# Kernel tuning notes

Hardware: AMD Instinct MI355X
Metric: run time of the kernel (lower is better)

The kernel has to match this reference:

```python
import jax, jax.numpy as jnp
import numpy as np

N_NODES = 50000
N_EDGES = 1_280_000
NODE_D = 13
EDGE_RAW_D = 1
H = 64
CONCAT_D = 2 * NODE_D + EDGE_RAW_D  # 27
NEG_SLOPE = 0.2


def _leaky(x):
    return jnp.where(x >= 0, x, NEG_SLOPE * x)


def _scatter_mean(vals, idx, num_nodes):
    # vals: [E, H]; idx: [E] int -> [num_nodes, H] mean over incident edges (0 if none)
    s = jax.ops.segment_sum(vals, idx, num_segments=num_nodes)
    cnt = jax.ops.segment_sum(jnp.ones((vals.shape[0], 1), vals.dtype), idx, num_segments=num_nodes)
    return s / jnp.maximum(cnt, 1.0)


def _conv(e, src, dst, num_nodes, w_self, b_self, w_in, w_out):
    h_self = e @ w_self + b_self
    agg_in = _scatter_mean(e, dst, num_nodes)[src]   # incoming-edge mean at src nodes
    agg_out = _scatter_mean(e, src, num_nodes)[dst]  # outgoing-edge mean at dst nodes
    return _leaky(h_self + agg_in @ w_in + agg_out @ w_out)


def setup_inputs() -> dict:
    key = jax.random.key(0)
    ks = jax.random.split(key, 24)

    def lin(k, fan_in, fan_out):
        return jax.random.normal(k, (fan_in, fan_out), jnp.float32) / np.sqrt(fan_in)

    inp = {
        'x': jax.random.normal(ks[0], (N_NODES, NODE_D), jnp.float32),
        'edge_index': jax.random.randint(ks[1], (2, N_EDGES), 0, N_NODES, jnp.int32),
        'raw_edge_attr': jax.random.normal(ks[2], (N_EDGES, EDGE_RAW_D), jnp.float32),
        'enc_w': lin(ks[3], CONCAT_D, H),
        'enc_b': jnp.zeros((H,), jnp.float32),
    }
    for i, base in zip((1, 2, 3), (4, 8, 12)):
        inp[f'w_self{i}'] = lin(ks[base], H, H)
        inp[f'b_self{i}'] = jnp.zeros((H,), jnp.float32)
        inp[f'w_in{i}'] = lin(ks[base + 1], H, H)
        inp[f'w_out{i}'] = lin(ks[base + 2], H, H)
    dims = [(H, 64), (64, 64), (64, 32), (32, 1)]
    for j, (fi, fo) in enumerate(dims, start=1):
        inp[f'mlp_w{j}'] = lin(ks[15 + j], fi, fo)
        inp[f'mlp_b{j}'] = jnp.zeros((fo,), jnp.float32)
    return inp


def reference(x, edge_index, raw_edge_attr, enc_w, enc_b,
              w_self1, b_self1, w_in1, w_out1,
              w_self2, b_self2, w_in2, w_out2,
              w_self3, b_self3, w_in3, w_out3,
              mlp_w1, mlp_b1, mlp_w2, mlp_b2, mlp_w3, mlp_b3, mlp_w4, mlp_b4):
    num_nodes = x.shape[0]
    src, dst = edge_index[0], edge_index[1]
    edge_attr = jnp.concatenate([x[src], x[dst], raw_edge_attr], axis=-1)  # [E, 27]
    h = _leaky(edge_attr @ enc_w + enc_b)
    h = _conv(h, src, dst, num_nodes, w_self1, b_self1, w_in1, w_out1)
    h = _conv(h, src, dst, num_nodes, w_self2, b_self2, w_in2, w_out2)
    h = _conv(h, src, dst, num_nodes, w_self3, b_self3, w_in3, w_out3)
    h = _leaky(h @ mlp_w1 + mlp_b1)
    h = _leaky(h @ mlp_w2 + mlp_b2)
    h = _leaky(h @ mlp_w3 + mlp_b3)
    return (h @ mlp_w4 + mlp_b4).squeeze(-1)  # [E]
```

## Files before the change

kernel.cpp:

```cpp
#include <hip/hip_runtime.h>


#define NN 50000
#define NNP 50048
#define NE 1280000
#define LDP 72
#define NB 196
#define NTILES 782
#define NPX 6250
#define CAP 64

#define WAVES 2
#define EDGE_ITERS 4
#define EDGE_BLOCKS 2500
#define ENC_ITERS 2
#define ENC_BLOCKS 5000

typedef unsigned int   u32;
typedef unsigned short u16;
typedef __attribute__((ext_vector_type(8))) short  short8;
typedef __attribute__((ext_vector_type(4))) float  floatx4;

#define MFMA16(a, b, c) __builtin_amdgcn_mfma_f32_16x16x32_bf16(a, b, c, 0, 0, 0)

__device__ __forceinline__ float lrelu(float x) { return fmaxf(x, 0.2f * x); }
__device__ __forceinline__ float bf2f(u16 u) { return __uint_as_float(((u32)u) << 16); }
__device__ __forceinline__ u16 f2bf(float f) {
    u32 b = __float_as_uint(f);
    return (u16)((b + 0x7FFFu + ((b >> 16) & 1u)) >> 16);
}
__device__ __forceinline__ u32 f2bf2(float lo, float hi) {
    u32 r;
    asm("v_cvt_pk_bf16_f32 %0, %1, %2" : "=v"(r) : "v"(lo), "v"(hi));
    return r;
}
__device__ __forceinline__ void ub2(u32 w, float& lo, float& hi) {
    lo = __uint_as_float(w << 16);
    hi = __uint_as_float(w & 0xFFFF0000u);
}

__device__ __forceinline__ short8 bfragP(const float* __restrict__ W, int ld, int n, int k0) {
    short8 b;
#pragma unroll
    for (int j = 0; j < 8; ++j) {
        const int p = k0 + j;
        const int k = (p & 3) * 16 + (p >> 2);
        b[j] = (short)f2bf(W[k * ld + n]);
    }
    return b;
}

__device__ __forceinline__ void mm_tile(const u16* __restrict__ tb,
                                        const short8 wf[2][4],
                                        floatx4 acc[4][4], int c16, int q4) {
#pragma unroll
    for (int mt = 0; mt < 4; ++mt) {
        const short8 a0 = *(const short8*)(tb + (mt * 16 + c16) * LDP + q4 * 8);
        const short8 a1 = *(const short8*)(tb + (mt * 16 + c16) * LDP + 32 + q4 * 8);
#pragma unroll
        for (int nt = 0; nt < 4; ++nt) {
            acc[mt][nt] = MFMA16(a0, wf[0][nt], acc[mt][nt]);
            acc[mt][nt] = MFMA16(a1, wf[1][nt], acc[mt][nt]);
        }
    }
}

__global__ void __launch_bounds__(256)
k_prep(const float* __restrict__ x, u16* __restrict__ xb)
{
    const int n = blockIdx.x * 256 + threadIdx.x;
    if (n >= NN) return;
    float f[13];
#pragma unroll
    for (int j = 0; j < 13; ++j) f[j] = x[n * 13 + j];
    uint4 p0, p1;
    p0.x = f2bf2(f[0],  f[1]);  p0.y = f2bf2(f[2],  f[3]);
    p0.z = f2bf2(f[4],  f[5]);  p0.w = f2bf2(f[6],  f[7]);
    p1.x = f2bf2(f[8],  f[9]);  p1.y = f2bf2(f[10], f[11]);
    p1.z = f2bf2(f[12], 0.0f);  p1.w = 0u;
    *(uint4*)(xb + (size_t)n * 16)     = p0;
    *(uint4*)(xb + (size_t)n * 16 + 8) = p1;
}

__global__ void __launch_bounds__(256)
k_fill(const int* __restrict__ ei, int* __restrict__ cnt_in, int* __restrict__ cnt_out,
       int* __restrict__ csr_in, int* __restrict__ csr_out)
{
    const int cls   = blockIdx.x & 7;
    const int slice = blockIdx.x >> 3;
    const int base  = (slice * 256 + threadIdx.x) * 8;
    const int lo = cls * NPX, hi = lo + NPX;
    int s[8], d[8];
#pragma unroll
    for (int k = 0; k < 8; ++k) s[k] = ei[base + k];
#pragma unroll
    for (int k = 0; k < 8; ++k) d[k] = ei[NE + base + k];
#pragma unroll
    for (int k = 0; k < 8; ++k)
        if (s[k] >= lo && s[k] < hi) {
            const int p = atomicAdd(&cnt_out[s[k]], 1);
            if (p < CAP) csr_out[s[k] * CAP + p] = base + k;
        }
#pragma unroll
    for (int k = 0; k < 8; ++k)
        if (d[k] >= lo && d[k] < hi) {
            const int q = atomicAdd(&cnt_in[d[k]], 1);
            if (q < CAP) csr_in[d[k] * CAP + q] = base + k;
        }
}

__global__ void __launch_bounds__(128)
k_enc(const u16* __restrict__ xb, const int* __restrict__ ei,
      const float* __restrict__ raw, const float* __restrict__ wenc,
      const float* __restrict__ benc, u16* __restrict__ hm)
{
    __shared__ int sidx[WAVES][64], didx[WAVES][64];
    const int w = threadIdx.x >> 6, lane = threadIdx.x & 63;
    const int c16 = lane & 15, q4 = lane >> 4;

    short8 wf[4];
    float bias[4];
#pragma unroll
    for (int nt = 0; nt < 4; ++nt) {
        short8 b;
#pragma unroll
        for (int j = 0; j < 8; ++j) {
            const int p = q4 * 8 + j;
            int row;
            if (p < 13)                 row = p;
            else if (p == 13)           row = 26;
            else if (p >= 16 && p < 29) row = 13 + (p - 16);
            else                        row = -1;
            b[j] = (short)(row >= 0 ? f2bf(wenc[row * 64 + nt * 16 + c16]) : 0);
        }
        wf[nt] = b;
        bias[nt] = benc[nt * 16 + c16];
    }

    for (int it = 0; it < ENC_ITERS; ++it) {
        const int tileId = (it * ENC_BLOCKS + blockIdx.x) * WAVES + w;
        const int e0 = tileId * 64;

        sidx[w][lane] = ei[e0 + lane];
        didx[w][lane] = ei[NE + e0 + lane];

#pragma unroll
        for (int mt = 0; mt < 4; ++mt) {
            const int arow = mt * 16 + c16;
            const int* nbase = (q4 < 2) ? sidx[w] : didx[w];
            const int node = nbase[arow];
            short8 a = *(const short8*)(xb + (size_t)node * 16 + (q4 & 1) * 8);
            const float rv = raw[e0 + arow];
            if (q4 == 1) a[5] = (short)(u16)f2bf2(rv, 0.0f);

            floatx4 acc[4];
#pragma unroll
            for (int nt = 0; nt < 4; ++nt) acc[nt] = (floatx4)(0.0f);
#pragma unroll
            for (int nt = 0; nt < 4; ++nt) acc[nt] = MFMA16(a, wf[nt], acc[nt]);
#pragma unroll
            for (int r = 0; r < 4; ++r) {
                const int rowi = mt * 16 + q4 * 4 + r;
                uint2 pkt;
                pkt.x = f2bf2(lrelu(acc[0][r] + bias[0]), lrelu(acc[1][r] + bias[1]));
                pkt.y = f2bf2(lrelu(acc[2][r] + bias[2]), lrelu(acc[3][r] + bias[3]));
                *(uint2*)(hm + (size_t)(e0 + rowi) * 64 + c16 * 4) = pkt;
            }
        }
    }
}

__global__ void __launch_bounds__(256)
k_mean(const u16* __restrict__ hm,
       const int* __restrict__ cnt_in, const int* __restrict__ csr_in,
       const int* __restrict__ cnt_out, const int* __restrict__ csr_out,
       u16* __restrict__ m_in, u16* __restrict__ m_out)
{
    const int w = threadIdx.x >> 6, lane = threadIdx.x & 63;
    const int node = blockIdx.x * 4 + w;
    const int rg = lane >> 3;
    const int co = (lane & 7) * 8;

    for (int pass = 0; pass < 2; ++pass) {
        const int* cnt = pass ? cnt_out : cnt_in;
        const int* csr = pass ? csr_out : csr_in;
        u16* mp        = pass ? m_out : m_in;

        const int deg = min(cnt[node], CAP);
        const int b0 = node * CAP, b1 = b0 + deg;
        float fa[8], fb[8];
#pragma unroll
        for (int c = 0; c < 8; ++c) { fa[c] = 0.f; fb[c] = 0.f; }

        int j = b0;
        for (; j + 16 <= b1; j += 16) {
            const int ea = csr[j + rg];
            const int eb = csr[j + 8 + rg];
            const uint4 va = *(const uint4*)(hm + (size_t)ea * 64 + co);
            const uint4 vb = *(const uint4*)(hm + (size_t)eb * 64 + co);
            float l0, h0, l1, h1, l2, h2, l3, h3;
            ub2(va.x, l0, h0); ub2(va.y, l1, h1); ub2(va.z, l2, h2); ub2(va.w, l3, h3);
            fa[0] += l0; fa[1] += h0; fa[2] += l1; fa[3] += h1;
            fa[4] += l2; fa[5] += h2; fa[6] += l3; fa[7] += h3;
            ub2(vb.x, l0, h0); ub2(vb.y, l1, h1); ub2(vb.z, l2, h2); ub2(vb.w, l3, h3);
            fb[0] += l0; fb[1] += h0; fb[2] += l1; fb[3] += h1;
            fb[4] += l2; fb[5] += h2; fb[6] += l3; fb[7] += h3;
        }
        for (; j < b1; j += 8) {
            const int jj = j + rg;
            const int idx = jj < b1 ? jj : b0;
            const float fl = jj < b1 ? 1.f : 0.f;
            const int e = csr[idx];
            const uint4 v = *(const uint4*)(hm + (size_t)e * 64 + co);
            float l0, h0, l1, h1, l2, h2, l3, h3;
            ub2(v.x, l0, h0); ub2(v.y, l1, h1); ub2(v.z, l2, h2); ub2(v.w, l3, h3);
            fa[0] += fl * l0; fa[1] += fl * h0; fa[2] += fl * l1; fa[3] += fl * h1;
            fa[4] += fl * l2; fa[5] += fl * h2; fa[6] += fl * l3; fa[7] += fl * h3;
        }
#pragma unroll
        for (int c = 0; c < 8; ++c) fa[c] += fb[c];
#pragma unroll
        for (int d = 8; d < 64; d <<= 1)
#pragma unroll
            for (int c = 0; c < 8; ++c) fa[c] += __shfl_xor(fa[c], d, 64);

        const float inv = 1.0f / (float)(deg > 0 ? deg : 1);
        if (lane < 8) {
            uint4 p;
            p.x = f2bf2(fa[0] * inv, fa[1] * inv);
            p.y = f2bf2(fa[2] * inv, fa[3] * inv);
            p.z = f2bf2(fa[4] * inv, fa[5] * inv);
            p.w = f2bf2(fa[6] * inv, fa[7] * inv);
            *(uint4*)(mp + (size_t)node * 64 + lane * 8) = p;
        }
    }
}

__global__ void __launch_bounds__(256)
k_nodemm(u16* t_in, u16* t_out,
         const float* __restrict__ w_in, const float* __restrict__ w_out)
{
    const int w = threadIdx.x >> 6, lane = threadIdx.x & 63;
    const int c16 = lane & 15, q4 = lane >> 4;
    const int tileId = blockIdx.x * 4 + w;
    if (tileId >= NTILES) return;
    const int n0 = tileId * 64;

    for (int pass = 0; pass < 2; ++pass) {
        u16* tp         = pass ? t_out : t_in;
        const float* wp = pass ? w_out : w_in;

        short8 wf[2][4];
#pragma unroll
        for (int ks = 0; ks < 2; ++ks)
#pragma unroll
            for (int nt = 0; nt < 4; ++nt)
                wf[ks][nt] = bfragP(wp, 64, nt * 16 + c16, ks * 32 + q4 * 8);

#pragma unroll
        for (int mt = 0; mt < 4; ++mt) {
            const short8* ap = (const short8*)(tp + (size_t)(n0 + mt * 16 + c16) * 64 + q4 * 8);
            const short8 a0 = ap[0];
            const short8 a1 = ap[4];
            floatx4 acc[4];
#pragma unroll
            for (int nt = 0; nt < 4; ++nt) acc[nt] = (floatx4)(0.0f);
#pragma unroll
            for (int nt = 0; nt < 4; ++nt) {
                acc[nt] = MFMA16(a0, wf[0][nt], acc[nt]);
                acc[nt] = MFMA16(a1, wf[1][nt], acc[nt]);
            }
#pragma unroll
            for (int r = 0; r < 4; ++r) {
                const int node = n0 + mt * 16 + q4 * 4 + r;
                if (node < NN) {
                    uint2 pkt;
                    pkt.x = f2bf2(acc[0][r], acc[1][r]);
                    pkt.y = f2bf2(acc[2][r], acc[3][r]);
                    *(uint2*)(tp + (size_t)node * 64 + c16 * 4) = pkt;
                }
            }
        }
    }
}

__global__ void __launch_bounds__(128, 4)
k_edge(const float* __restrict__ wself, const float* __restrict__ bself,
       const u16* __restrict__ t_in, const u16* __restrict__ t_out,
       const int* __restrict__ ei, u16* __restrict__ hm)
{
    __shared__ int sidx[WAVES][64], didx[WAVES][64];
    const int w = threadIdx.x >> 6, lane = threadIdx.x & 63;
    const int c16 = lane & 15, q4 = lane >> 4;

    short8 wf[2][4];
    float bias[4];
#pragma unroll
    for (int ks = 0; ks < 2; ++ks)
#pragma unroll
        for (int nt = 0; nt < 4; ++nt)
            wf[ks][nt] = bfragP(wself, 64, nt * 16 + c16, ks * 32 + q4 * 8);
#pragma unroll
    for (int nt = 0; nt < 4; ++nt) bias[nt] = bself[nt * 16 + c16];

    for (int it = 0; it < EDGE_ITERS; ++it) {
        const int tileId = (it * EDGE_BLOCKS + blockIdx.x) * WAVES + w;
        const int e0 = tileId * 64;
        sidx[w][lane] = ei[e0 + lane];
        didx[w][lane] = ei[NE + e0 + lane];

#pragma unroll
        for (int mt = 0; mt < 4; ++mt) {
            const short8* ap = (const short8*)(hm + (size_t)(e0 + mt * 16 + c16) * 64 + q4 * 8);
            const short8 a0 = ap[0];
            const short8 a1 = ap[4];
            floatx4 acc[4];
#pragma unroll
            for (int nt = 0; nt < 4; ++nt) acc[nt] = (floatx4)(0.0f);
#pragma unroll
            for (int nt = 0; nt < 4; ++nt) {
                acc[nt] = MFMA16(a0, wf[0][nt], acc[nt]);
                acc[nt] = MFMA16(a1, wf[1][nt], acc[nt]);
            }
            float tv[4][4], uv[4][4];
#pragma unroll
            for (int r = 0; r < 4; ++r) {
                const int s = sidx[w][mt * 16 + q4 * 4 + r];
                const uint2 v = *(const uint2*)(t_in + (size_t)s * 64 + c16 * 4);
                ub2(v.x, tv[r][0], tv[r][1]); ub2(v.y, tv[r][2], tv[r][3]);
            }
#pragma unroll
            for (int r = 0; r < 4; ++r) {
                const int d = didx[w][mt * 16 + q4 * 4 + r];
                const uint2 v = *(const uint2*)(t_out + (size_t)d * 64 + c16 * 4);
                ub2(v.x, uv[r][0], uv[r][1]); ub2(v.y, uv[r][2], uv[r][3]);
            }
#pragma unroll
            for (int r = 0; r < 4; ++r) {
                const int row = mt * 16 + q4 * 4 + r;
                const float v0 = lrelu(acc[0][r] + bias[0] + tv[r][0] + uv[r][0]);
                const float v1 = lrelu(acc[1][r] + bias[1] + tv[r][1] + uv[r][1]);
                const float v2 = lrelu(acc[2][r] + bias[2] + tv[r][2] + uv[r][2]);
                const float v3 = lrelu(acc[3][r] + bias[3] + tv[r][3] + uv[r][3]);
                uint2 pkt; pkt.x = f2bf2(v0, v1); pkt.y = f2bf2(v2, v3);
                *(uint2*)(hm + (size_t)(e0 + row) * 64 + c16 * 4) = pkt;
            }
        }
    }
}

__global__ void __launch_bounds__(128, 2)
k_edge_mlp(const float* __restrict__ wself, const float* __restrict__ bself,
           const u16* __restrict__ t_in, const u16* __restrict__ t_out,
           const int* __restrict__ ei, const u16* __restrict__ hm,
           const float* __restrict__ w1, const float* __restrict__ b1,
           const float* __restrict__ w2, const float* __restrict__ b2,
           const float* __restrict__ w3, const float* __restrict__ b3,
           const float* __restrict__ w4, const float* __restrict__ b4,
           float* __restrict__ out)
{
    __shared__ alignas(16) u16 tile[WAVES][64 * LDP];
    __shared__ int sidx[WAVES][64], didx[WAVES][64];
    const int w = threadIdx.x >> 6, lane = threadIdx.x & 63;
    const int c16 = lane & 15, q4 = lane >> 4;

    short8 wfS[2][4], wf1[2][4], wf2[2][4], wf3[2][2];
    float bS[4], bv1[4], bv2[4], bv3[2];
#pragma unroll
    for (int ks = 0; ks < 2; ++ks) {
#pragma unroll
        for (int nt = 0; nt < 4; ++nt) {
            wfS[ks][nt] = bfragP(wself, 64, nt * 16 + c16, ks * 32 + q4 * 8);
            wf1[ks][nt] = bfragP(w1,    64, nt * 16 + c16, ks * 32 + q4 * 8);
            wf2[ks][nt] = bfragP(w2,    64, nt * 16 + c16, ks * 32 + q4 * 8);
        }
#pragma unroll
        for (int nt = 0; nt < 2; ++nt)
            wf3[ks][nt] = bfragP(w3, 32, nt * 16 + c16, ks * 32 + q4 * 8);
    }
#pragma unroll
    for (int nt = 0; nt < 4; ++nt) { bS[nt] = bself[nt*16+c16]; bv1[nt] = b1[nt*16+c16]; bv2[nt] = b2[nt*16+c16]; }
#pragma unroll
    for (int nt = 0; nt < 2; ++nt) bv3[nt] = b3[nt * 16 + c16];
    const float w4a = w4[c16], w4b = w4[16 + c16], b4v = b4[0];

    for (int it = 0; it < EDGE_ITERS; ++it) {
        const int tileId = (it * EDGE_BLOCKS + blockIdx.x) * WAVES + w;
        const int e0 = tileId * 64;
        sidx[w][lane] = ei[e0 + lane];
        didx[w][lane] = ei[NE + e0 + lane];

#pragma unroll
        for (int mt = 0; mt < 4; ++mt) {
            const short8* ap = (const short8*)(hm + (size_t)(e0 + mt * 16 + c16) * 64 + q4 * 8);
            const short8 a0 = ap[0];
            const short8 a1 = ap[4];
            floatx4 acc[4];
#pragma unroll
            for (int nt = 0; nt < 4; ++nt) acc[nt] = (floatx4)(0.0f);
#pragma unroll
            for (int nt = 0; nt < 4; ++nt) {
                acc[nt] = MFMA16(a0, wfS[0][nt], acc[nt]);
                acc[nt] = MFMA16(a1, wfS[1][nt], acc[nt]);
            }
            float tv[4][4], uv[4][4];
#pragma unroll
            for (int r = 0; r < 4; ++r) {
                const int s = sidx[w][mt * 16 + q4 * 4 + r];
                const uint2 v = *(const uint2*)(t_in + (size_t)s * 64 + c16 * 4);
                ub2(v.x, tv[r][0], tv[r][1]); ub2(v.y, tv[r][2], tv[r][3]);
            }
#pragma unroll
            for (int r = 0; r < 4; ++r) {
                const int d = didx[w][mt * 16 + q4 * 4 + r];
                const uint2 v = *(const uint2*)(t_out + (size_t)d * 64 + c16 * 4);
                ub2(v.x, uv[r][0], uv[r][1]); ub2(v.y, uv[r][2], uv[r][3]);
            }
#pragma unroll
            for (int r = 0; r < 4; ++r) {
                const int row = mt * 16 + q4 * 4 + r;
                const float v0 = lrelu(acc[0][r] + bS[0] + tv[r][0] + uv[r][0]);
                const float v1 = lrelu(acc[1][r] + bS[1] + tv[r][1] + uv[r][1]);
                const float v2 = lrelu(acc[2][r] + bS[2] + tv[r][2] + uv[r][2]);
                const float v3 = lrelu(acc[3][r] + bS[3] + tv[r][3] + uv[r][3]);
                uint2 pkt; pkt.x = f2bf2(v0, v1); pkt.y = f2bf2(v2, v3);
                *(uint2*)(tile[w] + row * LDP + c16 * 4) = pkt;
            }
        }

        floatx4 acc[4][4];
#pragma unroll
        for (int mt = 0; mt < 4; ++mt)
#pragma unroll
            for (int nt = 0; nt < 4; ++nt) acc[mt][nt] = (floatx4)(0.0f);
        mm_tile(tile[w], wf1, acc, c16, q4);
#pragma unroll
        for (int mt = 0; mt < 4; ++mt)
#pragma unroll
            for (int r = 0; r < 4; ++r) {
                const int row = mt * 16 + q4 * 4 + r;
                uint2 pkt;
                pkt.x = f2bf2(lrelu(acc[mt][0][r] + bv1[0]), lrelu(acc[mt][1][r] + bv1[1]));
                pkt.y = f2bf2(lrelu(acc[mt][2][r] + bv1[2]), lrelu(acc[mt][3][r] + bv1[3]));
                *(uint2*)(tile[w] + row * LDP + c16 * 4) = pkt;
            }

#pragma unroll
        for (int mt = 0; mt < 4; ++mt)
#pragma unroll
            for (int nt = 0; nt < 4; ++nt) acc[mt][nt] = (floatx4)(0.0f);
        mm_tile(tile[w], wf2, acc, c16, q4);
#pragma unroll
        for (int mt = 0; mt < 4; ++mt)
#pragma unroll
            for (int r = 0; r < 4; ++r) {
                const int row = mt * 16 + q4 * 4 + r;
                uint2 pkt;
                pkt.x = f2bf2(lrelu(acc[mt][0][r] + bv2[0]), lrelu(acc[mt][1][r] + bv2[1]));
                pkt.y = f2bf2(lrelu(acc[mt][2][r] + bv2[2]), lrelu(acc[mt][3][r] + bv2[3]));
                *(uint2*)(tile[w] + row * LDP + c16 * 4) = pkt;
            }

        floatx4 a3[4][2];
#pragma unroll
        for (int mt = 0; mt < 4; ++mt)
#pragma unroll
            for (int nt = 0; nt < 2; ++nt) a3[mt][nt] = (floatx4)(0.0f);
#pragma unroll
        for (int mt = 0; mt < 4; ++mt) {
            const short8 a0 = *(const short8*)(tile[w] + (mt * 16 + c16) * LDP + q4 * 8);
            const short8 a1 = *(const short8*)(tile[w] + (mt * 16 + c16) * LDP + 32 + q4 * 8);
#pragma unroll
            for (int nt = 0; nt < 2; ++nt) {
                a3[mt][nt] = MFMA16(a0, wf3[0][nt], a3[mt][nt]);
                a3[mt][nt] = MFMA16(a1, wf3[1][nt], a3[mt][nt]);
            }
        }
#pragma unroll
        for (int mt = 0; mt < 4; ++mt)
#pragma unroll
            for (int r = 0; r < 4; ++r) {
                float p = lrelu(a3[mt][0][r] + bv3[0]) * w4a
                        + lrelu(a3[mt][1][r] + bv3[1]) * w4b;
                p += __shfl_xor(p, 1, 64);
                p += __shfl_xor(p, 2, 64);
                p += __shfl_xor(p, 4, 64);
                p += __shfl_xor(p, 8, 64);
                if (c16 == 0) out[e0 + mt * 16 + q4 * 4 + r] = p + b4v;
            }
    }
}

extern "C" void kernel_launch(void* const* d_in, const int* in_sizes, int n_in,
                              void* d_out, int out_size, void* d_ws, size_t ws_size,
                              hipStream_t stream)
{
    const float* x      = (const float*)d_in[0];
    const int*   ei     = (const int*)  d_in[1];
    const float* raw    = (const float*)d_in[2];
    const float* wenc   = (const float*)d_in[3];
    const float* benc   = (const float*)d_in[4];
    const float* wself1 = (const float*)d_in[5];
    const float* bself1 = (const float*)d_in[6];
    const float* win1   = (const float*)d_in[7];
    const float* wout1  = (const float*)d_in[8];
    const float* wself2 = (const float*)d_in[9];
    const float* bself2 = (const float*)d_in[10];
    const float* win2   = (const float*)d_in[11];
    const float* wout2  = (const float*)d_in[12];
    const float* wself3 = (const float*)d_in[13];
    const float* bself3 = (const float*)d_in[14];
    const float* win3   = (const float*)d_in[15];
    const float* wout3  = (const float*)d_in[16];
    const float* w1 = (const float*)d_in[17]; const float* b1 = (const float*)d_in[18];
    const float* w2 = (const float*)d_in[19]; const float* b2 = (const float*)d_in[20];
    const float* w3 = (const float*)d_in[21]; const float* b3 = (const float*)d_in[22];
    const float* w4 = (const float*)d_in[23]; const float* b4 = (const float*)d_in[24];

    u16*   t_in    = (u16*)d_ws;
    u16*   t_out   = t_in + (size_t)NNP * 64;
    int*   cnt_in  = (int*)(t_out + (size_t)NNP * 64);
    int*   cnt_out = cnt_in + NN;
    int*   csr_in  = cnt_out + NN;
    int*   csr_out = csr_in + (size_t)NN * CAP;
    u16*   hm      = (u16*)(csr_out + (size_t)NN * CAP);

    u16*   xb      = t_in;

    hipMemsetAsync(cnt_in, 0, (size_t)2 * NN * sizeof(int), stream);

    k_prep<<<NB, 256, 0, stream>>>(x, xb);

    k_fill<<<8 * (NE / 2048), 256, 0, stream>>>(ei, cnt_in, cnt_out, csr_in, csr_out);

    k_enc<<<ENC_BLOCKS, 128, 0, stream>>>(xb, ei, raw, wenc, benc, hm);

    for (int layer = 0; layer < 3; ++layer) {
        const float* wi = layer == 0 ? win1  : layer == 1 ? win2  : win3;
        const float* wo = layer == 0 ? wout1 : layer == 1 ? wout2 : wout3;
        k_mean<<<NN / 4, 256, 0, stream>>>(hm, cnt_in, csr_in, cnt_out, csr_out,
                                           t_in, t_out);
        k_nodemm<<<NB, 256, 0, stream>>>(t_in, t_out, wi, wo);
        if (layer == 0)
            k_edge<<<EDGE_BLOCKS, 128, 0, stream>>>(wself1, bself1, t_in, t_out, ei, hm);
        else if (layer == 1)
            k_edge<<<EDGE_BLOCKS, 128, 0, stream>>>(wself2, bself2, t_in, t_out, ei, hm);
        else
            k_edge_mlp<<<EDGE_BLOCKS, 128, 0, stream>>>(wself3, bself3, t_in, t_out, ei, hm,
                                                        w1, b1, w2, b2, w3, b3, w4, b4,
                                                        (float*)d_out);
    }
}
```

Measured before the change: 754.9 us.

## Fuse CSR adjacency build into encoder kernel and retune grid sizes

Removes the separate k_fill kernel and moves the atomic-counter CSR construction into k_enc, which already loads the src/dst indices for each 64-edge tile. This drops one launch and a second read of edge_index. It also drops the node-range partitioning that k_fill used to keep atomics local, so atomics now scatter across all nodes. Encoder and edge grid sizes are retuned to 2000 blocks with 5 iterations each.

Result: no change. 762.5 us (+1.0%).

```diff
diff --git a/kernel.cpp b/kernel.cpp
--- a/kernel.cpp
+++ b/kernel.cpp
@@ -7,14 +7,13 @@
 #define LDP 72
 #define NB 196
 #define NTILES 782
-#define NPX 6250
 #define CAP 64
 
 #define WAVES 2
-#define EDGE_ITERS 4
-#define EDGE_BLOCKS 2500
-#define ENC_ITERS 2
-#define ENC_BLOCKS 5000
+#define EDGE_ITERS 5
+#define EDGE_BLOCKS 2000
+#define ENC_ITERS 5
+#define ENC_BLOCKS 2000
 
 typedef unsigned int   u32;
 typedef unsigned short u16;
@@ -82,37 +81,12 @@
     *(uint4*)(xb + (size_t)n * 16 + 8) = p1;
 }
 
-__global__ void __launch_bounds__(256)
-k_fill(const int* __restrict__ ei, int* __restrict__ cnt_in, int* __restrict__ cnt_out,
-       int* __restrict__ csr_in, int* __restrict__ csr_out)
-{
-    const int cls   = blockIdx.x & 7;
-    const int slice = blockIdx.x >> 3;
-    const int base  = (slice * 256 + threadIdx.x) * 8;
-    const int lo = cls * NPX, hi = lo + NPX;
-    int s[8], d[8];
-#pragma unroll
-    for (int k = 0; k < 8; ++k) s[k] = ei[base + k];
-#pragma unroll
-    for (int k = 0; k < 8; ++k) d[k] = ei[NE + base + k];
-#pragma unroll
-    for (int k = 0; k < 8; ++k)
-        if (s[k] >= lo && s[k] < hi) {
-            const int p = atomicAdd(&cnt_out[s[k]], 1);
-            if (p < CAP) csr_out[s[k] * CAP + p] = base + k;
-        }
-#pragma unroll
-    for (int k = 0; k < 8; ++k)
-        if (d[k] >= lo && d[k] < hi) {
-            const int q = atomicAdd(&cnt_in[d[k]], 1);
-            if (q < CAP) csr_in[d[k] * CAP + q] = base + k;
-        }
-}
-
 __global__ void __launch_bounds__(128)
 k_enc(const u16* __restrict__ xb, const int* __restrict__ ei,
       const float* __restrict__ raw, const float* __restrict__ wenc,
-      const float* __restrict__ benc, u16* __restrict__ hm)
+      const float* __restrict__ benc, u16* __restrict__ hm,
+      int* __restrict__ cnt_in, int* __restrict__ cnt_out,
+      int* __restrict__ csr_in, int* __restrict__ csr_out)
 {
     __shared__ int sidx[WAVES][64], didx[WAVES][64];
     const int w = threadIdx.x >> 6, lane = threadIdx.x & 63;
@@ -141,8 +115,16 @@
         const int tileId = (it * ENC_BLOCKS + blockIdx.x) * WAVES + w;
         const int e0 = tileId * 64;
 
-        sidx[w][lane] = ei[e0 + lane];
-        didx[w][lane] = ei[NE + e0 + lane];
+        const int ms = ei[e0 + lane];
+        const int md = ei[NE + e0 + lane];
+        sidx[w][lane] = ms;
+        didx[w][lane] = md;
+
+        const int eidx = e0 + lane;
+        const int p = atomicAdd(&cnt_out[ms], 1);
+        if (p < CAP) csr_out[ms * CAP + p] = eidx;
+        const int q = atomicAdd(&cnt_in[md], 1);
+        if (q < CAP) csr_in[md * CAP + q] = eidx;
 
 #pragma unroll
         for (int mt = 0; mt < 4; ++mt) {
@@ -531,9 +513,8 @@
 
     k_prep<<<NB, 256, 0, stream>>>(x, xb);
 
-    k_fill<<<8 * (NE / 2048), 256, 0, stream>>>(ei, cnt_in, cnt_out, csr_in, csr_out);
-
-    k_enc<<<ENC_BLOCKS, 128, 0, stream>>>(xb, ei, raw, wenc, benc, hm);
+    k_enc<<<ENC_BLOCKS, 128, 0, stream>>>(xb, ei, raw, wenc, benc, hm,
+                                          cnt_in, cnt_out, csr_in, csr_out);
 
     for (int layer = 0; layer < 3; ++layer) {
         const float* wi = layer == 0 ? win1  : layer == 1 ? win2  : win3;
```
